# Kernel tuning notes

Hardware: AMD Instinct MI355X
Metric: run time of the kernel (lower is better)

The kernel has to match this reference:

```python
import jax, jax.numpy as jnp
import numpy as np

B, S, D_MODEL = 2, 2048, 2048
H, KVH, HD = 32, 8, 64
N_REP = H // KVH
EPS = 1e-6


def _rope_tables(seq_len, head_dim):
    pos = np.arange(seq_len, dtype=np.float32)
    inv_freq = 1.0 / (10000.0 ** (np.arange(0, head_dim, 2, dtype=np.float32) / head_dim))
    freqs = pos[:, None] * inv_freq[None, :]           # [S, HD/2]
    emb = np.concatenate([freqs, freqs], axis=-1)      # [S, HD]
    return jnp.asarray(np.cos(emb)), jnp.asarray(np.sin(emb))


def setup_inputs() -> dict:
    key = jax.random.key(0)
    ks = jax.random.split(key, 6)
    x = jax.random.normal(ks[0], (B, S, D_MODEL), jnp.float32)
    rope_cos, rope_sin = _rope_tables(S, HD)
    sc_in = 1.0 / np.sqrt(D_MODEL).astype(np.float32)
    sc_o = 1.0 / np.sqrt(H * HD).astype(np.float32)
    Wq = jax.random.normal(ks[1], (H * HD, D_MODEL), jnp.float32) * sc_in
    Wk = jax.random.normal(ks[2], (KVH * HD, D_MODEL), jnp.float32) * sc_in
    Wv = jax.random.normal(ks[3], (KVH * HD, D_MODEL), jnp.float32) * sc_in
    Wo = jax.random.normal(ks[4], (D_MODEL, H * HD), jnp.float32) * sc_o
    q_norm_w = jnp.ones((HD,), jnp.float32)
    k_norm_w = jnp.ones((HD,), jnp.float32)
    return dict(x=x, rope_cos=rope_cos, rope_sin=rope_sin, Wq=Wq, Wk=Wk, Wv=Wv,
                Wo=Wo, q_norm_w=q_norm_w, k_norm_w=k_norm_w)


def _rms_norm(x, w):
    return x * jax.lax.rsqrt(jnp.mean(x * x, axis=-1, keepdims=True) + EPS) * w


def _rotate_half(x):
    x1, x2 = jnp.split(x, 2, axis=-1)
    return jnp.concatenate((-x2, x1), axis=-1)


def reference(x, rope_cos, rope_sin, Wq, Wk, Wv, Wo, q_norm_w, k_norm_w):
    b, s, _ = x.shape
    q = (x @ Wq.T).reshape(b, s, H, HD)
    k = (x @ Wk.T).reshape(b, s, KVH, HD)
    v = (x @ Wv.T).reshape(b, s, KVH, HD)
    # per-head QK RMSNorm
    q = _rms_norm(q, q_norm_w)
    k = _rms_norm(k, k_norm_w)
    # RoPE: cos/sin [S, HD] -> broadcast over heads
    cos = rope_cos[:, None, :]
    sin = rope_sin[:, None, :]
    q = q * cos + _rotate_half(q) * sin
    k = k * cos + _rotate_half(k) * sin
    # GQA: repeat_interleave KV heads
    k = jnp.repeat(k, N_REP, axis=2)
    v = jnp.repeat(v, N_REP, axis=2)
    q = q.transpose(0, 2, 1, 3)  # [B,H,S,HD]
    k = k.transpose(0, 2, 1, 3)
    v = v.transpose(0, 2, 1, 3)
    scale = np.float32(1.0 / np.sqrt(HD))
    scores = jnp.einsum('bhqd,bhkd->bhqk', q, k) * scale
    causal = jnp.tril(jnp.ones((s, s), dtype=bool))
    scores = jnp.where(causal, scores, jnp.finfo(scores.dtype).min)
    attn = jax.nn.softmax(scores, axis=-1)
    out = jnp.einsum('bhqk,bhkd->bhqd', attn, v)
    out = out.transpose(0, 2, 1, 3).reshape(b, s, H * HD)
    return out @ Wo.T
```

## Files before the change

kernel.cpp:

```cpp
#include <hip/hip_runtime.h>
#include <stdint.h>

#define B_ 2
#define S_ 2048
#define DM_ 2048
#define H_ 32
#define KVH_ 8
#define HD_ 64
#define NQK_ 3072

typedef unsigned short u16;
typedef unsigned int u32;
typedef __attribute__((ext_vector_type(8))) short bf16x8;
typedef __attribute__((ext_vector_type(4))) float f32x4;

static __device__ __forceinline__ u16 f2bf(float f) {
  unsigned int u = __float_as_uint(f);
  u = (u + 0x7fffu + ((u >> 16) & 1u)) >> 16;
  return (u16)u;
}
static __device__ __forceinline__ float bf2f(u16 v) {
  unsigned int u = ((unsigned int)v) << 16;
  return __uint_as_float(u);
}

static __device__ __forceinline__ void gload16(const void* g, void* lds_wave_base) {
  __builtin_amdgcn_global_load_lds(
      (__attribute__((address_space(1))) unsigned int*)(uintptr_t)g,
      (__attribute__((address_space(3))) unsigned int*)(uintptr_t)lds_wave_base,
      16, 0, 0);
}

__global__ void cvt_bf16(const float* __restrict__ in, u16* __restrict__ out, int n4) {
  int i = blockIdx.x * blockDim.x + threadIdx.x;
  if (i >= n4) return;
  const float4 v = ((const float4*)in)[i];
  ushort4 o;
  o.x = f2bf(v.x); o.y = f2bf(v.y); o.z = f2bf(v.z); o.w = f2bf(v.w);
  ((ushort4*)out)[i] = o;
}

#define BM 128
#define BN 128
#define BK 32

#define GEMM_BODY(CSTORE)                                                       \
  __shared__ u16 As[2][BM * BK];                                                \
  __shared__ u16 Bs[2][BN * BK];                                                \
  const int t = threadIdx.x;                                                    \
  const int lane = t & 63;                                                      \
  const int w = t >> 6;                                                         \
  const int wr = (w >> 1) * 64, wc = (w & 1) * 64;                              \
  const int m0 = blockIdx.y * BM;                                               \
  const int n0 = blockIdx.x * BN;                                               \
  f32x4 acc[4][4] = {};                                                         \
  const char* Ab = (const char*)A;                                              \
  const char* Bb = (const char*)Bw;                                             \
  const size_t K2 = (size_t)K * 2;                                              \
  const int P0 = t * 16;                                                        \
  const int row0 = P0 >> 6, kb0 = P0 & 63;                                      \
  const int P1 = 4096 + t * 16;                                                 \
  const int row1 = P1 >> 6, kb1 = P1 & 63;                                      \
  const int Pb0 = (w << 10), Pb1 = 4096 + (w << 10);                            \
  auto STAGE = [&](int buf, int k0) {                                           \
    gload16(Ab + (size_t)(m0 + row0) * K2 + (size_t)k0 * 2 + kb0, (char*)As[buf] + Pb0); \
    gload16(Ab + (size_t)(m0 + row1) * K2 + (size_t)k0 * 2 + kb1, (char*)As[buf] + Pb1); \
    gload16(Bb + (size_t)(n0 + row0) * K2 + (size_t)k0 * 2 + kb0, (char*)Bs[buf] + Pb0); \
    gload16(Bb + (size_t)(n0 + row1) * K2 + (size_t)k0 * 2 + kb1, (char*)Bs[buf] + Pb1); \
  };                                                                            \
  STAGE(0, 0);                                                                  \
  __syncthreads();                                                              \
  int cur = 0;                                                                  \
  for (int k0 = 0; k0 < K; k0 += BK) {                                          \
    if (k0 + BK < K) STAGE(cur ^ 1, k0 + BK);                                   \
    bf16x8 af[4], bfr[4];                                                       \
    _Pragma("unroll")                                                           \
    for (int m = 0; m < 4; m++)                                                 \
      af[m] = *(const bf16x8*)((const char*)As[cur] +                           \
               (wr + m * 16 + (lane & 15)) * 64 + ((lane >> 4) << 4));          \
    _Pragma("unroll")                                                           \
    for (int n = 0; n < 4; n++)                                                 \
      bfr[n] = *(const bf16x8*)((const char*)Bs[cur] +                          \
               (wc + n * 16 + (lane & 15)) * 64 + ((lane >> 4) << 4));          \
    _Pragma("unroll")                                                           \
    for (int m = 0; m < 4; m++)                                                 \
      _Pragma("unroll")                                                         \
      for (int n = 0; n < 4; n++)                                               \
        acc[m][n] = __builtin_amdgcn_mfma_f32_16x16x32_bf16(af[m], bfr[n], acc[m][n], 0, 0, 0); \
    __syncthreads();                                                            \
    cur ^= 1;                                                                   \
  }                                                                             \
  _Pragma("unroll")                                                             \
  for (int m = 0; m < 4; m++) {                                                 \
    const int r0 = m0 + wr + m * 16 + ((lane >> 4) << 2);                       \
    _Pragma("unroll")                                                           \
    for (int n = 0; n < 4; n++) {                                               \
      const int c = n0 + wc + n * 16 + (lane & 15);                             \
      _Pragma("unroll")                                                         \
      for (int j = 0; j < 4; j++) CSTORE;                                       \
    }                                                                           \
  }

__global__ __launch_bounds__(256) void gemm_bt(const u16* __restrict__ A,
                                               const u16* __restrict__ Bw,
                                               float* __restrict__ C,
                                               int M, int N, int K) {
  GEMM_BODY(C[(size_t)(r0 + j) * N + c] = acc[m][n][j])
}

__global__ __launch_bounds__(256) void gemm_btb(const u16* __restrict__ A,
                                                const u16* __restrict__ Bw,
                                                u16* __restrict__ C,
                                                int M, int N, int K) {
  GEMM_BODY(C[(size_t)(r0 + j) * N + c] = f2bf(acc[m][n][j]))
}

__global__ void norm_rope_inplace(u16* __restrict__ QKV, const float* __restrict__ cosT,
                                  const float* __restrict__ sinT,
                                  const float* __restrict__ qw,
                                  const float* __restrict__ kw, float qscale) {
  const int r = blockIdx.x * 4 + (threadIdx.x >> 6);
  const int lane = threadIdx.x & 63;
  const int hh2 = r % 40;
  const int bs = r / 40;
  const int s = bs & (S_ - 1);
  const bool isq = hh2 < 32;
  u16* p = QKV + (size_t)bs * NQK_ + hh2 * 64 + lane;
  float x = bf2f(*p);
  float ss = x * x;
#pragma unroll
  for (int m = 1; m < 64; m <<= 1) ss += __shfl_xor(ss, m, 64);
  const float wgt = isq ? qw[lane] : kw[lane];
  float xn = x * rsqrtf(ss * (1.0f / 64.0f) + 1e-6f) * wgt;
  float pr = __shfl_xor(xn, 32, 64);
  float o = xn * cosT[s * 64 + lane] + (lane < 32 ? -pr : pr) * sinT[s * 64 + lane];
  *p = f2bf(o * (isq ? qscale : 1.0f));
}

__global__ void v_transpose(const u16* __restrict__ QKV, u16* __restrict__ Vt) {
  __shared__ u16 tile[64][72];
  const int s0 = blockIdx.x * 64;
  const int bk = blockIdx.y;
  const int b = bk / KVH_, kvh = bk % KVH_;
  const int t = threadIdx.x;
#pragma unroll
  for (int it = 0; it < 16; it++) {
    int idx = it * 256 + t;
    int sl = idx >> 6, d = idx & 63;
    tile[sl][d] = QKV[(size_t)(b * S_ + s0 + sl) * NQK_ + 2560 + kvh * 64 + d];
  }
  __syncthreads();
#pragma unroll
  for (int it = 0; it < 16; it++) {
    int idx = it * 256 + t;
    int d = idx >> 6, sl = idx & 63;
    Vt[(((size_t)(b * KVH_ + kvh)) * HD_ + d) * S_ + s0 + sl] = tile[sl][d];
  }
}

__global__ __launch_bounds__(256, 4) void attn_fwd(const u16* __restrict__ QKV,
                                                   const u16* __restrict__ Vt,
                                                   u16* __restrict__ Out) {
  __shared__ u16 Ksm[2][64 * 64];
  __shared__ u16 Vsm[2][64 * 64];
  __shared__ u16 Psm[4][16 * 64];

  const int t = threadIdx.x, lane = t & 63, w = t >> 6;
  const int q = lane & 15, g = lane >> 4;

  const int fid = blockIdx.y * 16 + blockIdx.x;
  const int xcd = fid & 7, slot = fid >> 3;
  const int kg = xcd * 2 + (slot >> 6);
  const int sub = slot & 63;
  const int ip = sub >> 2;
  const int b = kg >> 3, kvh = kg & 7;
  const int h = kvh * 4 + (sub & 3);

  const char* Kb = (const char*)(QKV + (size_t)b * S_ * NQK_ + 2048 + kvh * 64);
  const char* Vb = (const char*)(Vt + ((size_t)(b * KVH_ + kvh)) * HD_ * S_);

  const int SP0 = t * 16, SP1 = 4096 + t * 16;
  const int srow0 = SP0 >> 7, scb0 = (SP0 ^ ((srow0 & 7) << 4)) & 127;
  const int srow1 = SP1 >> 7, scb1 = (SP1 ^ ((srow1 & 7) << 4)) & 127;
  const int SB0 = (w << 10), SB1 = 4096 + (w << 10);
  const size_t KROW = (size_t)NQK_ * 2;

  auto STAGE = [&](int buf, int kt) {
    gload16(Kb + (size_t)(kt * 64 + srow0) * KROW + scb0, (char*)Ksm[buf] + SB0);
    gload16(Kb + (size_t)(kt * 64 + srow1) * KROW + scb1, (char*)Ksm[buf] + SB1);
    gload16(Vb + (size_t)srow0 * (S_ * 2) + (size_t)kt * 128 + scb0, (char*)Vsm[buf] + SB0);
    gload16(Vb + (size_t)srow1 * (S_ * 2) + (size_t)kt * 128 + scb1, (char*)Vsm[buf] + SB1);
  };

  const int swz = (q & 7) << 4;
  int koff[4][2], voff[4][2], pwoff[4][2], proff[2];
#pragma unroll
  for (int nt = 0; nt < 4; nt++)
#pragma unroll
    for (int hh = 0; hh < 2; hh++) {
      koff[nt][hh] = ((nt * 16 + q) * 128 + hh * 64 + g * 16) ^ swz;
      voff[nt][hh] = ((nt * 16 + q) * 128 + hh * 64 + g * 16) ^ swz;
      pwoff[nt][hh] = (q * 128 + nt * 32 + g * 8 + hh * 4) ^ swz;
    }
#pragma unroll
  for (int c = 0; c < 2; c++) proff[c] = (q * 128 + c * 64 + g * 16) ^ swz;

  bf16x8 ones;
#pragma unroll
  for (int j = 0; j < 8; j++) ones[j] = (short)0x3F80;

  auto process = [&](int qt) {
    const int q0w = qt * 64 + w * 16;
    bf16x8 aq[2];
    {
      const u16* qp = QKV + (size_t)(b * S_ + q0w + q) * NQK_ + h * 64 + g * 8;
      aq[0] = *(const bf16x8*)qp;
      aq[1] = *(const bf16x8*)(qp + 32);
    }
    f32x4 o_acc[4] = {};
    f32x4 l_acc = {};
    float m_i = -1e30f;

    STAGE(0, 0);
    __syncthreads();
    int cur = 0;

    for (int kt = 0; kt <= qt; kt++) {
      if (kt < qt) STAGE(cur ^ 1, kt + 1);

      f32x4 sc[4];
      __builtin_amdgcn_s_setprio(1);
#pragma unroll
      for (int nt = 0; nt < 4; nt++) {
        f32x4 s = {};
#pragma unroll
        for (int hh = 0; hh < 2; hh++) {
          bf16x8 bk = *(const bf16x8*)((const char*)Ksm[cur] + koff[nt][hh]);
          s = __builtin_amdgcn_mfma_f32_16x16x32_bf16(bk, aq[hh], s, 0, 0, 0);
        }
        sc[nt] = s;
      }
      __builtin_amdgcn_s_setprio(0);

      if (kt == qt) {
#pragma unroll
        for (int nt = 0; nt < 4; nt++)
#pragma unroll
          for (int r = 0; r < 4; r++)
            if (nt * 16 + g * 4 + r > w * 16 + q) sc[nt][r] = -1e30f;
      }

      float mx;
      {
        float m0 = fmaxf(fmaxf(sc[0][0], sc[0][1]), fmaxf(sc[0][2], sc[0][3]));
        float m1 = fmaxf(fmaxf(sc[1][0], sc[1][1]), fmaxf(sc[1][2], sc[1][3]));
        float m2 = fmaxf(fmaxf(sc[2][0], sc[2][1]), fmaxf(sc[2][2], sc[2][3]));
        float m3 = fmaxf(fmaxf(sc[3][0], sc[3][1]), fmaxf(sc[3][2], sc[3][3]));
        mx = fmaxf(fmaxf(m0, m1), fmaxf(m2, m3));
      }
      mx = fmaxf(mx, __shfl_xor(mx, 16, 64));
      mx = fmaxf(mx, __shfl_xor(mx, 32, 64));

      if (!__all(mx <= m_i + 8.0f)) {
        const float mn = fmaxf(m_i, mx);
        const float a = exp2f(m_i - mn);
        m_i = mn;
        float aT[4];
#pragma unroll
        for (int r = 0; r < 4; r++)
          aT[r] = __shfl(a, (lane & 48) + ((lane & 48) >> 2) + r, 64);
#pragma unroll
        for (int r = 0; r < 4; r++) {
          l_acc[r] *= aT[r];
#pragma unroll
          for (int dt = 0; dt < 4; dt++) o_acc[dt][r] *= aT[r];
        }
      }

#pragma unroll
      for (int nt = 0; nt < 4; nt++)
#pragma unroll
        for (int r = 0; r < 4; r++) sc[nt][r] = exp2f(sc[nt][r] - m_i);
#pragma unroll
      for (int nt = 0; nt < 4; nt++)
#pragma unroll
        for (int hh = 0; hh < 2; hh++) {
          u32 wv;
          asm("v_cvt_pk_bf16_f32 %0, %1, %2"
              : "=v"(wv) : "v"(sc[nt][2 * hh]), "v"(sc[nt][2 * hh + 1]));
          *(u32*)((char*)Psm[w] + pwoff[nt][hh]) = wv;
        }

      asm volatile("s_waitcnt lgkmcnt(0)" ::: "memory");
      __builtin_amdgcn_sched_barrier(0);

      bf16x8 pa[2];
#pragma unroll
      for (int c = 0; c < 2; c++)
        pa[c] = *(const bf16x8*)((const char*)Psm[w] + proff[c]);

      __builtin_amdgcn_s_setprio(1);
      l_acc = __builtin_amdgcn_mfma_f32_16x16x32_bf16(pa[0], ones, l_acc, 0, 0, 0);
      l_acc = __builtin_amdgcn_mfma_f32_16x16x32_bf16(pa[1], ones, l_acc, 0, 0, 0);
#pragma unroll
      for (int c = 0; c < 2; c++)
#pragma unroll
        for (int dt = 0; dt < 4; dt++) {
          bf16x8 bv = *(const bf16x8*)((const char*)Vsm[cur] + voff[dt][c]);
          o_acc[dt] = __builtin_amdgcn_mfma_f32_16x16x32_bf16(pa[c], bv, o_acc[dt], 0, 0, 0);
        }
      __builtin_amdgcn_s_setprio(0);

      __syncthreads();
      cur ^= 1;
    }

#pragma unroll
    for (int r = 0; r < 4; r++) {
      const int qg = q0w + g * 4 + r;
      const float inv = 1.0f / l_acc[r];
#pragma unroll
      for (int dt = 0; dt < 4; dt++)
        Out[(((size_t)b * S_ + qg) * H_ + h) * HD_ + dt * 16 + q] =
            f2bf(o_acc[dt][r] * inv);
    }
  };

  process(ip);
  process(31 - ip);
}

extern "C" void kernel_launch(void* const* d_in, const int* in_sizes, int n_in,
                              void* d_out, int out_size, void* d_ws, size_t ws_size,
                              hipStream_t stream) {
  const float* x  = (const float*)d_in[0];
  const float* rc = (const float*)d_in[1];
  const float* rs = (const float*)d_in[2];
  const float* Wq = (const float*)d_in[3];
  const float* Wk = (const float*)d_in[4];
  const float* Wv = (const float*)d_in[5];
  const float* Wo = (const float*)d_in[6];
  const float* qw = (const float*)d_in[7];
  const float* kw = (const float*)d_in[8];
  float* out = (float*)d_out;

  char* ws = (char*)d_ws;
  const size_t MB = (size_t)1 << 20;
  u16* xb   = (u16*)(ws + 0 * MB);
  u16* wbq  = (u16*)(ws + 16 * MB);
  u16* QKVb = (u16*)(ws + 28 * MB);
  u16* Vtb  = (u16*)(ws + 52 * MB);
  u16* AO   = xb;

  const int MT = B_ * S_;
  const float QSC = 0.125f * 1.44269504089f;

  cvt_bf16<<<dim3(MT * DM_ / 1024), 256, 0, stream>>>(x, xb, MT * DM_ / 4);
  cvt_bf16<<<dim3(DM_ * DM_ / 1024), 256, 0, stream>>>(Wq, wbq, DM_ * DM_ / 4);
  cvt_bf16<<<dim3(512 * DM_ / 1024), 256, 0, stream>>>(Wk, wbq + (size_t)DM_ * DM_, 512 * DM_ / 4);
  cvt_bf16<<<dim3(512 * DM_ / 1024), 256, 0, stream>>>(Wv, wbq + (size_t)DM_ * DM_ + (size_t)512 * DM_, 512 * DM_ / 4);

  gemm_btb<<<dim3(NQK_ / BN, MT / BM), 256, 0, stream>>>(xb, wbq, QKVb, MT, NQK_, DM_);

  norm_rope_inplace<<<dim3(MT * 40 / 4), 256, 0, stream>>>(QKVb, rc, rs, qw, kw, QSC);

  v_transpose<<<dim3(S_ / 64, B_ * KVH_), 256, 0, stream>>>(QKVb, Vtb);

  attn_fwd<<<dim3(16, 64), 256, 0, stream>>>(QKVb, Vtb, AO);

  cvt_bf16<<<dim3(DM_ * DM_ / 1024), 256, 0, stream>>>(Wo, wbq, DM_ * DM_ / 4);
  gemm_bt<<<dim3(DM_ / BN, MT / BM), 256, 0, stream>>>(AO, wbq, out, MT, DM_, DM_);
}
```

Before: 240.1 us.

## Restructure attention to 32x32 MFMA with paired lo/hi query tiles sharing K/V loads

The attention kernel now uses 32x32x16 MFMAs, giving each wave 32 query rows instead of 16. Each block processes a low and a high causal query tile together in one pass, so every staged K/V tile serves both. The P matrix is rearranged in registers with v_permlane32_swap instead of a round trip through LDS. The grid shrinks to 512 blocks with launch bounds of 2, trading occupancy and register pressure for fewer K/V loads and no LDS traffic for P.

```diff
diff --git a/kernel.cpp b/kernel.cpp
--- a/kernel.cpp
+++ b/kernel.cpp
@@ -13,6 +13,8 @@
 typedef unsigned int u32;
 typedef __attribute__((ext_vector_type(8))) short bf16x8;
 typedef __attribute__((ext_vector_type(4))) float f32x4;
+typedef __attribute__((ext_vector_type(16))) float f32x16;
+typedef __attribute__((ext_vector_type(4))) u32 u32x4;
 
 static __device__ __forceinline__ u16 f2bf(float f) {
   unsigned int u = __float_as_uint(f);
@@ -158,23 +160,28 @@
   }
 }
 
-__global__ __launch_bounds__(256, 4) void attn_fwd(const u16* __restrict__ QKV,
+__global__ __launch_bounds__(256, 2) void attn_fwd(const u16* __restrict__ QKV,
                                                    const u16* __restrict__ Vt,
                                                    u16* __restrict__ Out) {
   __shared__ u16 Ksm[2][64 * 64];
   __shared__ u16 Vsm[2][64 * 64];
-  __shared__ u16 Psm[4][16 * 64];
 
   const int t = threadIdx.x, lane = t & 63, w = t >> 6;
-  const int q = lane & 15, g = lane >> 4;
-
-  const int fid = blockIdx.y * 16 + blockIdx.x;
+  const int q31 = lane & 31, hi = lane >> 5;
+
+  const int fid = blockIdx.x;
   const int xcd = fid & 7, slot = fid >> 3;
-  const int kg = xcd * 2 + (slot >> 6);
-  const int sub = slot & 63;
-  const int ip = sub >> 2;
+  const int kg = xcd * 2 + (slot >> 5);
+  const int sub = slot & 31;
   const int b = kg >> 3, kvh = kg & 7;
   const int h = kvh * 4 + (sub & 3);
+  const int ip = sub >> 2;
+
+  const int qlo0 = ip * 128 + w * 32;
+  const int qhi0 = (15 - ip) * 128 + w * 32;
+  const int ktlo_max = (qlo0 + 31) >> 6;
+  const int kthi_max = (qhi0 + 31) >> 6;
+  const int KT = (15 - ip) * 2 + 1;
 
   const char* Kb = (const char*)(QKV + (size_t)b * S_ * NQK_ + 2048 + kvh * 64);
   const char* Vb = (const char*)(Vt + ((size_t)(b * KVH_ + kvh)) * HD_ * S_);
@@ -192,142 +199,169 @@
     gload16(Vb + (size_t)srow1 * (S_ * 2) + (size_t)kt * 128 + scb1, (char*)Vsm[buf] + SB1);
   };
 
-  const int swz = (q & 7) << 4;
-  int koff[4][2], voff[4][2], pwoff[4][2], proff[2];
-#pragma unroll
-  for (int nt = 0; nt < 4; nt++)
-#pragma unroll
-    for (int hh = 0; hh < 2; hh++) {
-      koff[nt][hh] = ((nt * 16 + q) * 128 + hh * 64 + g * 16) ^ swz;
-      voff[nt][hh] = ((nt * 16 + q) * 128 + hh * 64 + g * 16) ^ swz;
-      pwoff[nt][hh] = (q * 128 + nt * 32 + g * 8 + hh * 4) ^ swz;
-    }
-#pragma unroll
-  for (int c = 0; c < 2; c++) proff[c] = (q * 128 + c * 64 + g * 16) ^ swz;
+  bf16x8 qf0[4], qf1[4];
+  {
+    const u16* qp0 = QKV + (size_t)(b * S_ + qlo0 + q31) * NQK_ + h * 64 + hi * 8;
+    const u16* qp1 = QKV + (size_t)(b * S_ + qhi0 + q31) * NQK_ + h * 64 + hi * 8;
+#pragma unroll
+    for (int sl = 0; sl < 4; sl++) {
+      qf0[sl] = *(const bf16x8*)(qp0 + sl * 16);
+      qf1[sl] = *(const bf16x8*)(qp1 + sl * 16);
+    }
+  }
 
   bf16x8 ones;
 #pragma unroll
   for (int j = 0; j < 8; j++) ones[j] = (short)0x3F80;
 
-  auto process = [&](int qt) {
-    const int q0w = qt * 64 + w * 16;
-    bf16x8 aq[2];
+  f32x16 o00 = {}, o01 = {}, o10 = {}, o11 = {};
+  f32x16 l0 = {}, l1 = {};
+  float m0 = -1e30f, m1 = -1e30f;
+
+  auto cvtpk = [](float a, float bb) {
+    u32 r;
+    asm("v_cvt_pk_bf16_f32 %0, %1, %2" : "=v"(r) : "v"(a), "v"(bb));
+    return r;
+  };
+
+  STAGE(0, 0);
+  __syncthreads();
+  int cur = 0;
+
+  for (int kt = 0; kt <= KT; kt++) {
+    if (kt < KT) STAGE(cur ^ 1, kt + 1);
+
+    bf16x8 kf[2][4];
+#pragma unroll
+    for (int kh = 0; kh < 2; kh++)
+#pragma unroll
+      for (int sl = 0; sl < 4; sl++) {
+        const int row = kh * 32 + q31;
+        const int byt = (row * 128 + sl * 32 + hi * 16) ^ ((row & 7) << 4);
+        kf[kh][sl] = *(const bf16x8*)((const char*)Ksm[cur] + byt);
+      }
+
+    bf16x8 pa0[4], pa1[4];
+    const bool act0 = (kt <= ktlo_max);
+    const bool act1 = (kt <= kthi_max);
+
+#define QTILE(ACT, QF, PA, MI, LI, OA, OB, Q0, KTMAX)                           \
+    if (ACT) {                                                                  \
+      f32x16 p0 = {}, p1 = {};                                                  \
+      __builtin_amdgcn_s_setprio(1);                                            \
+      _Pragma("unroll")                                                         \
+      for (int sl = 0; sl < 4; sl++) {                                          \
+        p0 = __builtin_amdgcn_mfma_f32_32x32x16_bf16(kf[0][sl], QF[sl], p0, 0, 0, 0); \
+        p1 = __builtin_amdgcn_mfma_f32_32x32x16_bf16(kf[1][sl], QF[sl], p1, 0, 0, 0); \
+      }                                                                         \
+      __builtin_amdgcn_s_setprio(0);                                            \
+      if (kt == KTMAX) {                                                        \
+        const int qg = Q0 + q31;                                                \
+        _Pragma("unroll")                                                       \
+        for (int r = 0; r < 16; r++) {                                          \
+          const int crow = (r & 3) + 8 * (r >> 2) + 4 * hi;                     \
+          if (kt * 64 + crow > qg) p0[r] = -1e30f;                              \
+          if (kt * 64 + 32 + crow > qg) p1[r] = -1e30f;                         \
+        }                                                                       \
+      }                                                                         \
+      float mx = fmaxf(p0[0], p1[0]);                                           \
+      _Pragma("unroll")                                                         \
+      for (int r = 1; r < 16; r++) mx = fmaxf(mx, fmaxf(p0[r], p1[r]));         \
+      mx = fmaxf(mx, __shfl_xor(mx, 32, 64));                                   \
+      if (!__all(mx <= MI + 8.0f)) {                                            \
+        const float mn = fmaxf(MI, mx);                                         \
+        const float al = exp2f(MI - mn);                                        \
+        MI = mn;                                                                \
+        _Pragma("unroll")                                                       \
+        for (int r = 0; r < 16; r++) {                                          \
+          const float aO = __shfl(al, (r & 3) + 8 * (r >> 2) + 4 * hi, 64);     \
+          LI[r] *= aO; OA[r] *= aO; OB[r] *= aO;                                \
+        }                                                                       \
+      }                                                                         \
+      _Pragma("unroll")                                                         \
+      for (int r = 0; r < 16; r++) {                                            \
+        p0[r] = exp2f(p0[r] - MI);                                              \
+        p1[r] = exp2f(p1[r] - MI);                                              \
+      }                                                                         \
+      u32 wa, wb2, wc2, wd;                                                     \
+      union { u32x4 u; bf16x8 h; } cv;                                          \
+      wa = cvtpk(p0[0], p0[1]);  wb2 = cvtpk(p0[2], p0[3]);                     \
+      wc2 = cvtpk(p0[4], p0[5]); wd = cvtpk(p0[6], p0[7]);                      \
+      asm("v_permlane32_swap_b32 %0, %1" : "+v"(wa), "+v"(wc2));                \
+      asm("v_permlane32_swap_b32 %0, %1" : "+v"(wb2), "+v"(wd));                \
+      cv.u[0] = wa; cv.u[1] = wb2; cv.u[2] = wc2; cv.u[3] = wd; PA[0] = cv.h;   \
+      wa = cvtpk(p0[8], p0[9]);   wb2 = cvtpk(p0[10], p0[11]);                  \
+      wc2 = cvtpk(p0[12], p0[13]); wd = cvtpk(p0[14], p0[15]);                  \
+      asm("v_permlane32_swap_b32 %0, %1" : "+v"(wa), "+v"(wc2));                \
+      asm("v_permlane32_swap_b32 %0, %1" : "+v"(wb2), "+v"(wd));                \
+      cv.u[0] = wa; cv.u[1] = wb2; cv.u[2] = wc2; cv.u[3] = wd; PA[1] = cv.h;   \
+      wa = cvtpk(p1[0], p1[1]);  wb2 = cvtpk(p1[2], p1[3]);                     \
+      wc2 = cvtpk(p1[4], p1[5]); wd = cvtpk(p1[6], p1[7]);                      \
+      asm("v_permlane32_swap_b32 %0, %1" : "+v"(wa), "+v"(wc2));                \
+      asm("v_permlane32_swap_b32 %0, %1" : "+v"(wb2), "+v"(wd));                \
+      cv.u[0] = wa; cv.u[1] = wb2; cv.u[2] = wc2; cv.u[3] = wd; PA[2] = cv.h;   \
+      wa = cvtpk(p1[8], p1[9]);   wb2 = cvtpk(p1[10], p1[11]);                  \
+      wc2 = cvtpk(p1[12], p1[13]); wd = cvtpk(p1[14], p1[15]);                  \
+      asm("v_permlane32_swap_b32 %0, %1" : "+v"(wa), "+v"(wc2));                \
+      asm("v_permlane32_swap_b32 %0, %1" : "+v"(wb2), "+v"(wd));                \
+      cv.u[0] = wa; cv.u[1] = wb2; cv.u[2] = wc2; cv.u[3] = wd; PA[3] = cv.h;   \
+    }
+
+    QTILE(act0, qf0, pa0, m0, l0, o00, o01, qlo0, ktlo_max)
+    QTILE(act1, qf1, pa1, m1, l1, o10, o11, qhi0, kthi_max)
+#undef QTILE
+
+    bf16x8 vf[4][2];
+#pragma unroll
+    for (int sl = 0; sl < 4; sl++)
+#pragma unroll
+      for (int dt = 0; dt < 2; dt++) {
+        const int row = dt * 32 + q31;
+        const int byt = (row * 128 + sl * 32 + hi * 16) ^ ((row & 7) << 4);
+        vf[sl][dt] = *(const bf16x8*)((const char*)Vsm[cur] + byt);
+      }
+
+    __builtin_amdgcn_s_setprio(1);
+    if (act0) {
+#pragma unroll
+      for (int sl = 0; sl < 4; sl++) {
+        l0 = __builtin_amdgcn_mfma_f32_32x32x16_bf16(pa0[sl], ones, l0, 0, 0, 0);
+        o00 = __builtin_amdgcn_mfma_f32_32x32x16_bf16(pa0[sl], vf[sl][0], o00, 0, 0, 0);
+        o01 = __builtin_amdgcn_mfma_f32_32x32x16_bf16(pa0[sl], vf[sl][1], o01, 0, 0, 0);
+      }
+    }
+    if (act1) {
+#pragma unroll
+      for (int sl = 0; sl < 4; sl++) {
+        l1 = __builtin_amdgcn_mfma_f32_32x32x16_bf16(pa1[sl], ones, l1, 0, 0, 0);
+        o10 = __builtin_amdgcn_mfma_f32_32x32x16_bf16(pa1[sl], vf[sl][0], o10, 0, 0, 0);
+        o11 = __builtin_amdgcn_mfma_f32_32x32x16_bf16(pa1[sl], vf[sl][1], o11, 0, 0, 0);
+      }
+    }
+    __builtin_amdgcn_s_setprio(0);
+
+    __syncthreads();
+    cur ^= 1;
+  }
+
+#pragma unroll
+  for (int r = 0; r < 16; r++) {
+    const int crow = (r & 3) + 8 * (r >> 2) + 4 * hi;
     {
-      const u16* qp = QKV + (size_t)(b * S_ + q0w + q) * NQK_ + h * 64 + g * 8;
-      aq[0] = *(const bf16x8*)qp;
-      aq[1] = *(const bf16x8*)(qp + 32);
-    }
-    f32x4 o_acc[4] = {};
-    f32x4 l_acc = {};
-    float m_i = -1e30f;
-
-    STAGE(0, 0);
-    __syncthreads();
-    int cur = 0;
-
-    for (int kt = 0; kt <= qt; kt++) {
-      if (kt < qt) STAGE(cur ^ 1, kt + 1);
-
-      f32x4 sc[4];
-      __builtin_amdgcn_s_setprio(1);
-#pragma unroll
-      for (int nt = 0; nt < 4; nt++) {
-        f32x4 s = {};
-#pragma unroll
-        for (int hh = 0; hh < 2; hh++) {
-          bf16x8 bk = *(const bf16x8*)((const char*)Ksm[cur] + koff[nt][hh]);
-          s = __builtin_amdgcn_mfma_f32_16x16x32_bf16(bk, aq[hh], s, 0, 0, 0);
-        }
-        sc[nt] = s;
-      }
-      __builtin_amdgcn_s_setprio(0);
-
-      if (kt == qt) {
-#pragma unroll
-        for (int nt = 0; nt < 4; nt++)
-#pragma unroll
-          for (int r = 0; r < 4; r++)
-            if (nt * 16 + g * 4 + r > w * 16 + q) sc[nt][r] = -1e30f;
-      }
-
-      float mx;
-      {
-        float m0 = fmaxf(fmaxf(sc[0][0], sc[0][1]), fmaxf(sc[0][2], sc[0][3]));
-        float m1 = fmaxf(fmaxf(sc[1][0], sc[1][1]), fmaxf(sc[1][2], sc[1][3]));
-        float m2 = fmaxf(fmaxf(sc[2][0], sc[2][1]), fmaxf(sc[2][2], sc[2][3]));
-        float m3 = fmaxf(fmaxf(sc[3][0], sc[3][1]), fmaxf(sc[3][2], sc[3][3]));
-        mx = fmaxf(fmaxf(m0, m1), fmaxf(m2, m3));
-      }
-      mx = fmaxf(mx, __shfl_xor(mx, 16, 64));
-      mx = fmaxf(mx, __shfl_xor(mx, 32, 64));
-
-      if (!__all(mx <= m_i + 8.0f)) {
-        const float mn = fmaxf(m_i, mx);
-        const float a = exp2f(m_i - mn);
-        m_i = mn;
-        float aT[4];
-#pragma unroll
-        for (int r = 0; r < 4; r++)
-          aT[r] = __shfl(a, (lane & 48) + ((lane & 48) >> 2) + r, 64);
-#pragma unroll
-        for (int r = 0; r < 4; r++) {
-          l_acc[r] *= aT[r];
-#pragma unroll
-          for (int dt = 0; dt < 4; dt++) o_acc[dt][r] *= aT[r];
-        }
-      }
-
-#pragma unroll
-      for (int nt = 0; nt < 4; nt++)
-#pragma unroll
-        for (int r = 0; r < 4; r++) sc[nt][r] = exp2f(sc[nt][r] - m_i);
-#pragma unroll
-      for (int nt = 0; nt < 4; nt++)
-#pragma unroll
-        for (int hh = 0; hh < 2; hh++) {
-          u32 wv;
-          asm("v_cvt_pk_bf16_f32 %0, %1, %2"
-              : "=v"(wv) : "v"(sc[nt][2 * hh]), "v"(sc[nt][2 * hh + 1]));
-          *(u32*)((char*)Psm[w] + pwoff[nt][hh]) = wv;
-        }
-
-      asm volatile("s_waitcnt lgkmcnt(0)" ::: "memory");
-      __builtin_amdgcn_sched_barrier(0);
-
-      bf16x8 pa[2];
-#pragma unroll
-      for (int c = 0; c < 2; c++)
-        pa[c] = *(const bf16x8*)((const char*)Psm[w] + proff[c]);
-
-      __builtin_amdgcn_s_setprio(1);
-      l_acc = __builtin_amdgcn_mfma_f32_16x16x32_bf16(pa[0], ones, l_acc, 0, 0, 0);
-      l_acc = __builtin_amdgcn_mfma_f32_16x16x32_bf16(pa[1], ones, l_acc, 0, 0, 0);
-#pragma unroll
-      for (int c = 0; c < 2; c++)
-#pragma unroll
-        for (int dt = 0; dt < 4; dt++) {
-          bf16x8 bv = *(const bf16x8*)((const char*)Vsm[cur] + voff[dt][c]);
-          o_acc[dt] = __builtin_amdgcn_mfma_f32_16x16x32_bf16(pa[c], bv, o_acc[dt], 0, 0, 0);
-        }
-      __builtin_amdgcn_s_setprio(0);
-
-      __syncthreads();
-      cur ^= 1;
-    }
-
-#pragma unroll
-    for (int r = 0; r < 4; r++) {
-      const int qg = q0w + g * 4 + r;
-      const float inv = 1.0f / l_acc[r];
-#pragma unroll
-      for (int dt = 0; dt < 4; dt++)
-        Out[(((size_t)b * S_ + qg) * H_ + h) * HD_ + dt * 16 + q] =
-            f2bf(o_acc[dt][r] * inv);
-    }
-  };
-
-  process(ip);
-  process(31 - ip);
+      const int qg = qlo0 + crow;
+      const float inv = 1.0f / l0[r];
+      u16* op = Out + (((size_t)(b * S_ + qg)) * H_ + h) * HD_;
+      op[q31] = f2bf(o00[r] * inv);
+      op[32 + q31] = f2bf(o01[r] * inv);
+    }
+    {
+      const int qg = qhi0 + crow;
+      const float inv = 1.0f / l1[r];
+      u16* op = Out + (((size_t)(b * S_ + qg)) * H_ + h) * HD_;
+      op[q31] = f2bf(o10[r] * inv);
+      op[32 + q31] = f2bf(o11[r] * inv);
+    }
+  }
 }
 
 extern "C" void kernel_launch(void* const* d_in, const int* in_sizes, int n_in,
@@ -366,7 +400,7 @@
 
   v_transpose<<<dim3(S_ / 64, B_ * KVH_), 256, 0, stream>>>(QKVb, Vtb);
 
-  attn_fwd<<<dim3(16, 64), 256, 0, stream>>>(QKVb, Vtb, AO);
+  attn_fwd<<<dim3(512), 256, 0, stream>>>(QKVb, Vtb, AO);
 
   cvt_bf16<<<dim3(DM_ * DM_ / 1024), 256, 0, stream>>>(Wo, wbq, DM_ * DM_ / 4);
   gemm_bt<<<dim3(DM_ / BN, MT / BM), 256, 0, stream>>>(AO, wbq, out, MT, DM_, DM_);
```

Result: no change. 240.3 us (+0.1%).

## Rewrite attention with 32x32 MFMA, split-KV waves and register-resident P

Applied to the files above, without the earlier changes.

The attention kernel moves from 16x16x32 to 32x32x16 MFMAs, with each wave owning a 32-row query tile and half of each 64-key block (two waves per query tile split along keys). P is converted to the MFMA operand layout in registers using v_permlane32_swap instead of a round trip through LDS, and row sums are computed with shuffles instead of a ones-MFMA. The two key-halves are merged at the end through shared memory. Each block now handles one query slab instead of a paired short+long slab, so the grid doubles and load balancing relies on scheduling longest slabs first. This trades an extra end-of-block reduction and half-idle waves on the diagonal block for fewer LDS operations and larger MFMA tiles.

```diff
diff --git a/kernel.cpp b/kernel.cpp
--- a/kernel.cpp
+++ b/kernel.cpp
@@ -13,6 +13,8 @@
 typedef unsigned int u32;
 typedef __attribute__((ext_vector_type(8))) short bf16x8;
 typedef __attribute__((ext_vector_type(4))) float f32x4;
+typedef __attribute__((ext_vector_type(16))) float f32x16;
+typedef __attribute__((ext_vector_type(4))) u32 u32x4;
 
 static __device__ __forceinline__ u16 f2bf(float f) {
   unsigned int u = __float_as_uint(f);
@@ -163,18 +165,21 @@
                                                    u16* __restrict__ Out) {
   __shared__ u16 Ksm[2][64 * 64];
   __shared__ u16 Vsm[2][64 * 64];
-  __shared__ u16 Psm[4][16 * 64];
 
   const int t = threadIdx.x, lane = t & 63, w = t >> 6;
-  const int q = lane & 15, g = lane >> 4;
-
-  const int fid = blockIdx.y * 16 + blockIdx.x;
+  const int q31 = lane & 31, hi = lane >> 5;
+  const int tile_r = w & 1, kside = w >> 1;
+
+  const int fid = blockIdx.x;
   const int xcd = fid & 7, slot = fid >> 3;
-  const int kg = xcd * 2 + (slot >> 6);
-  const int sub = slot & 63;
-  const int ip = sub >> 2;
+  const int kg = xcd * 2 + (slot >> 7);
+  const int sub = slot & 127;
   const int b = kg >> 3, kvh = kg & 7;
   const int h = kvh * 4 + (sub & 3);
+  const int slab = 31 - (sub >> 2);
+
+  const int q0 = slab * 64 + tile_r * 32;
+  const int KTM = slab;
 
   const char* Kb = (const char*)(QKV + (size_t)b * S_ * NQK_ + 2048 + kvh * 64);
   const char* Vb = (const char*)(Vt + ((size_t)(b * KVH_ + kvh)) * HD_ * S_);
@@ -192,142 +197,146 @@
     gload16(Vb + (size_t)srow1 * (S_ * 2) + (size_t)kt * 128 + scb1, (char*)Vsm[buf] + SB1);
   };
 
-  const int swz = (q & 7) << 4;
-  int koff[4][2], voff[4][2], pwoff[4][2], proff[2];
-#pragma unroll
-  for (int nt = 0; nt < 4; nt++)
-#pragma unroll
-    for (int hh = 0; hh < 2; hh++) {
-      koff[nt][hh] = ((nt * 16 + q) * 128 + hh * 64 + g * 16) ^ swz;
-      voff[nt][hh] = ((nt * 16 + q) * 128 + hh * 64 + g * 16) ^ swz;
-      pwoff[nt][hh] = (q * 128 + nt * 32 + g * 8 + hh * 4) ^ swz;
-    }
-#pragma unroll
-  for (int c = 0; c < 2; c++) proff[c] = (q * 128 + c * 64 + g * 16) ^ swz;
-
-  bf16x8 ones;
-#pragma unroll
-  for (int j = 0; j < 8; j++) ones[j] = (short)0x3F80;
-
-  auto process = [&](int qt) {
-    const int q0w = qt * 64 + w * 16;
-    bf16x8 aq[2];
-    {
-      const u16* qp = QKV + (size_t)(b * S_ + q0w + q) * NQK_ + h * 64 + g * 8;
-      aq[0] = *(const bf16x8*)qp;
-      aq[1] = *(const bf16x8*)(qp + 32);
-    }
-    f32x4 o_acc[4] = {};
-    f32x4 l_acc = {};
-    float m_i = -1e30f;
-
-    STAGE(0, 0);
-    __syncthreads();
-    int cur = 0;
-
-    for (int kt = 0; kt <= qt; kt++) {
-      if (kt < qt) STAGE(cur ^ 1, kt + 1);
-
-      f32x4 sc[4];
+  STAGE(0, 0);
+
+  bf16x8 qf[4];
+  {
+    const u16* qp = QKV + (size_t)(b * S_ + q0 + q31) * NQK_ + h * 64 + hi * 8;
+#pragma unroll
+    for (int sl = 0; sl < 4; sl++) qf[sl] = *(const bf16x8*)(qp + sl * 16);
+  }
+
+  f32x16 o0 = {}, o1 = {};
+  float m_i = -1e30f, l_i = 0.0f;
+
+  auto cvtpk = [](float a, float bb) {
+    u32 r;
+    asm("v_cvt_pk_bf16_f32 %0, %1, %2" : "=v"(r) : "v"(a), "v"(bb));
+    return r;
+  };
+
+  const int swz = (q31 & 7) << 4;
+  __syncthreads();
+  int cur = 0;
+
+  for (int kt = 0; kt <= KTM; kt++) {
+    if (kt < KTM) STAGE(cur ^ 1, kt + 1);
+
+    const bool act = (kt < KTM) || (kside <= tile_r);
+    if (act) {
+      f32x16 p = {};
       __builtin_amdgcn_s_setprio(1);
 #pragma unroll
-      for (int nt = 0; nt < 4; nt++) {
-        f32x4 s = {};
-#pragma unroll
-        for (int hh = 0; hh < 2; hh++) {
-          bf16x8 bk = *(const bf16x8*)((const char*)Ksm[cur] + koff[nt][hh]);
-          s = __builtin_amdgcn_mfma_f32_16x16x32_bf16(bk, aq[hh], s, 0, 0, 0);
+      for (int sl = 0; sl < 4; sl++) {
+        const int byt = ((kside * 32 + q31) * 128 + sl * 32 + hi * 16) ^ swz;
+        bf16x8 kf = *(const bf16x8*)((const char*)Ksm[cur] + byt);
+        p = __builtin_amdgcn_mfma_f32_32x32x16_bf16(kf, qf[sl], p, 0, 0, 0);
+      }
+      __builtin_amdgcn_s_setprio(0);
+
+      if (kt == KTM) {
+        const int rel = tile_r * 32 + q31 - kside * 32;
+#pragma unroll
+        for (int r = 0; r < 16; r++) {
+          const int crow = (r & 3) + 8 * (r >> 2) + 4 * hi;
+          if (crow > rel) p[r] = -1e30f;
         }
-        sc[nt] = s;
-      }
-      __builtin_amdgcn_s_setprio(0);
-
-      if (kt == qt) {
-#pragma unroll
-        for (int nt = 0; nt < 4; nt++)
-#pragma unroll
-          for (int r = 0; r < 4; r++)
-            if (nt * 16 + g * 4 + r > w * 16 + q) sc[nt][r] = -1e30f;
-      }
-
-      float mx;
-      {
-        float m0 = fmaxf(fmaxf(sc[0][0], sc[0][1]), fmaxf(sc[0][2], sc[0][3]));
-        float m1 = fmaxf(fmaxf(sc[1][0], sc[1][1]), fmaxf(sc[1][2], sc[1][3]));
-        float m2 = fmaxf(fmaxf(sc[2][0], sc[2][1]), fmaxf(sc[2][2], sc[2][3]));
-        float m3 = fmaxf(fmaxf(sc[3][0], sc[3][1]), fmaxf(sc[3][2], sc[3][3]));
-        mx = fmaxf(fmaxf(m0, m1), fmaxf(m2, m3));
-      }
-      mx = fmaxf(mx, __shfl_xor(mx, 16, 64));
+      }
+
+      float a0 = fmaxf(p[0], p[1]),  a1 = fmaxf(p[2], p[3]);
+      float a2 = fmaxf(p[4], p[5]),  a3 = fmaxf(p[6], p[7]);
+      float a4 = fmaxf(p[8], p[9]),  a5 = fmaxf(p[10], p[11]);
+      float a6 = fmaxf(p[12], p[13]), a7 = fmaxf(p[14], p[15]);
+      float mx = fmaxf(fmaxf(fmaxf(a0, a1), fmaxf(a2, a3)),
+                       fmaxf(fmaxf(a4, a5), fmaxf(a6, a7)));
       mx = fmaxf(mx, __shfl_xor(mx, 32, 64));
 
       if (!__all(mx <= m_i + 8.0f)) {
         const float mn = fmaxf(m_i, mx);
-        const float a = exp2f(m_i - mn);
+        const float al = exp2f(m_i - mn);
         m_i = mn;
-        float aT[4];
-#pragma unroll
-        for (int r = 0; r < 4; r++)
-          aT[r] = __shfl(a, (lane & 48) + ((lane & 48) >> 2) + r, 64);
-#pragma unroll
-        for (int r = 0; r < 4; r++) {
-          l_acc[r] *= aT[r];
-#pragma unroll
-          for (int dt = 0; dt < 4; dt++) o_acc[dt][r] *= aT[r];
+        l_i *= al;
+#pragma unroll
+        for (int r = 0; r < 16; r++) {
+          const float aO = __shfl(al, (r & 3) + 8 * (r >> 2) + 4 * hi, 64);
+          o0[r] *= aO;
+          o1[r] *= aO;
         }
       }
 
-#pragma unroll
-      for (int nt = 0; nt < 4; nt++)
-#pragma unroll
-        for (int r = 0; r < 4; r++) sc[nt][r] = exp2f(sc[nt][r] - m_i);
-#pragma unroll
-      for (int nt = 0; nt < 4; nt++)
-#pragma unroll
-        for (int hh = 0; hh < 2; hh++) {
-          u32 wv;
-          asm("v_cvt_pk_bf16_f32 %0, %1, %2"
-              : "=v"(wv) : "v"(sc[nt][2 * hh]), "v"(sc[nt][2 * hh + 1]));
-          *(u32*)((char*)Psm[w] + pwoff[nt][hh]) = wv;
-        }
-
-      asm volatile("s_waitcnt lgkmcnt(0)" ::: "memory");
-      __builtin_amdgcn_sched_barrier(0);
+      float rs = 0.0f;
+#pragma unroll
+      for (int r = 0; r < 16; r++) {
+        p[r] = exp2f(p[r] - m_i);
+        rs += p[r];
+      }
+      rs += __shfl_xor(rs, 32, 64);
+      l_i += rs;
 
       bf16x8 pa[2];
-#pragma unroll
-      for (int c = 0; c < 2; c++)
-        pa[c] = *(const bf16x8*)((const char*)Psm[w] + proff[c]);
+      {
+        u32 wa, wb2, wc2, wd;
+        union { u32x4 u; bf16x8 hh; } cv;
+        wa = cvtpk(p[0], p[1]);   wb2 = cvtpk(p[2], p[3]);
+        wc2 = cvtpk(p[4], p[5]);  wd = cvtpk(p[6], p[7]);
+        asm("v_permlane32_swap_b32 %0, %1" : "+v"(wa), "+v"(wc2));
+        asm("v_permlane32_swap_b32 %0, %1" : "+v"(wb2), "+v"(wd));
+        cv.u[0] = wa; cv.u[1] = wb2; cv.u[2] = wc2; cv.u[3] = wd; pa[0] = cv.hh;
+        wa = cvtpk(p[8], p[9]);    wb2 = cvtpk(p[10], p[11]);
+        wc2 = cvtpk(p[12], p[13]); wd = cvtpk(p[14], p[15]);
+        asm("v_permlane32_swap_b32 %0, %1" : "+v"(wa), "+v"(wc2));
+        asm("v_permlane32_swap_b32 %0, %1" : "+v"(wb2), "+v"(wd));
+        cv.u[0] = wa; cv.u[1] = wb2; cv.u[2] = wc2; cv.u[3] = wd; pa[1] = cv.hh;
+      }
 
       __builtin_amdgcn_s_setprio(1);
-      l_acc = __builtin_amdgcn_mfma_f32_16x16x32_bf16(pa[0], ones, l_acc, 0, 0, 0);
-      l_acc = __builtin_amdgcn_mfma_f32_16x16x32_bf16(pa[1], ones, l_acc, 0, 0, 0);
-#pragma unroll
-      for (int c = 0; c < 2; c++)
-#pragma unroll
-        for (int dt = 0; dt < 4; dt++) {
-          bf16x8 bv = *(const bf16x8*)((const char*)Vsm[cur] + voff[dt][c]);
-          o_acc[dt] = __builtin_amdgcn_mfma_f32_16x16x32_bf16(pa[c], bv, o_acc[dt], 0, 0, 0);
-        }
+#pragma unroll
+      for (int j = 0; j < 2; j++) {
+        const int colb = kside * 64 + j * 32 + hi * 16;
+        bf16x8 v0 = *(const bf16x8*)((const char*)Vsm[cur] +
+                     ((q31 * 128 + colb) ^ swz));
+        bf16x8 v1 = *(const bf16x8*)((const char*)Vsm[cur] +
+                     (((32 + q31) * 128 + colb) ^ swz));
+        o0 = __builtin_amdgcn_mfma_f32_32x32x16_bf16(pa[j], v0, o0, 0, 0, 0);
+        o1 = __builtin_amdgcn_mfma_f32_32x32x16_bf16(pa[j], v1, o1, 0, 0, 0);
+      }
       __builtin_amdgcn_s_setprio(0);
-
-      __syncthreads();
-      cur ^= 1;
     }
 
-#pragma unroll
-    for (int r = 0; r < 4; r++) {
-      const int qg = q0w + g * 4 + r;
-      const float inv = 1.0f / l_acc[r];
-#pragma unroll
-      for (int dt = 0; dt < 4; dt++)
-        Out[(((size_t)b * S_ + qg) * H_ + h) * HD_ + dt * 16 + q] =
-            f2bf(o_acc[dt][r] * inv);
+    __syncthreads();
+    cur ^= 1;
+  }
+
+  float* smo = (float*)Ksm;
+  float* smlm = (float*)Vsm;
+  if (kside == 1) {
+    float* dst = smo + tile_r * 2048 + lane * 32;
+#pragma unroll
+    for (int r = 0; r < 16; r++) { dst[r] = o0[r]; dst[16 + r] = o1[r]; }
+    smlm[tile_r * 128 + lane * 2] = l_i;
+    smlm[tile_r * 128 + lane * 2 + 1] = m_i;
+  }
+  __syncthreads();
+  if (kside == 0) {
+    const float lB = smlm[tile_r * 128 + lane * 2];
+    const float mB = smlm[tile_r * 128 + lane * 2 + 1];
+    const float m12 = fmaxf(m_i, mB);
+    const float aA = exp2f(m_i - m12);
+    const float aB = exp2f(mB - m12);
+    const float linv = 1.0f / (l_i * aA + lB * aB);
+    const float* src = smo + tile_r * 2048 + lane * 32;
+#pragma unroll
+    for (int r = 0; r < 16; r++) {
+      const int crow = (r & 3) + 8 * (r >> 2) + 4 * hi;
+      const float fA = __shfl(aA, crow, 64);
+      const float fB = __shfl(aB, crow, 64);
+      const float fl = __shfl(linv, crow, 64);
+      const int qg = q0 + crow;
+      u16* op = Out + (((size_t)(b * S_ + qg)) * H_ + h) * HD_;
+      op[q31] = f2bf((o0[r] * fA + src[r] * fB) * fl);
+      op[32 + q31] = f2bf((o1[r] * fA + src[16 + r] * fB) * fl);
     }
-  };
-
-  process(ip);
-  process(31 - ip);
+  }
 }
 
 extern "C" void kernel_launch(void* const* d_in, const int* in_sizes, int n_in,
@@ -366,7 +375,7 @@
 
   v_transpose<<<dim3(S_ / 64, B_ * KVH_), 256, 0, stream>>>(QKVb, Vtb);
 
-  attn_fwd<<<dim3(16, 64), 256, 0, stream>>>(QKVb, Vtb, AO);
+  attn_fwd<<<dim3(2048), 256, 0, stream>>>(QKVb, Vtb, AO);
 
   cvt_bf16<<<dim3(DM_ * DM_ / 1024), 256, 0, stream>>>(Wo, wbq, DM_ * DM_ / 4);
   gemm_bt<<<dim3(DM_ / BN, MT / BM), 256, 0, stream>>>(AO, wbq, out, MT, DM_, DM_);
```

Result: slower. 247.4 us (+3.0%).

## Replace GEMM with 128x256 tile, 8-wave, triple-buffered swizzled LDS pipeline

Applied to the files above, without the earlier changes.

Replaces the double-buffered 128x128x32 GEMM with a 512-thread kernel that computes 128x256 tiles with BK=64. It uses three LDS buffers with XOR-swizzled rows to avoid bank conflicts, explicit vmcnt waits and barriers to interleave prefetch with MFMA quadrants, s_setprio around the MFMA blocks, and an XCD-aware block remapping. The aim is higher arithmetic intensity and better overlap of global loads with MFMA in the QKV and output projections. In exchange the kernel hardcodes K=2048, uses about 144KB of LDS, and its hand-scheduled waitcnt logic is fragile.

```diff
diff --git a/kernel.cpp b/kernel.cpp
--- a/kernel.cpp
+++ b/kernel.cpp
@@ -8,6 +8,8 @@
 #define KVH_ 8
 #define HD_ 64
 #define NQK_ 3072
+#define GK 2048
+#define NT 32
 
 typedef unsigned short u16;
 typedef unsigned int u32;
@@ -40,79 +42,126 @@
   ((ushort4*)out)[i] = o;
 }
 
-#define BM 128
-#define BN 128
-#define BK 32
-
-#define GEMM_BODY(CSTORE)                                                       \
-  __shared__ u16 As[2][BM * BK];                                                \
-  __shared__ u16 Bs[2][BN * BK];                                                \
-  const int t = threadIdx.x;                                                    \
-  const int lane = t & 63;                                                      \
-  const int w = t >> 6;                                                         \
-  const int wr = (w >> 1) * 64, wc = (w & 1) * 64;                              \
-  const int m0 = blockIdx.y * BM;                                               \
-  const int n0 = blockIdx.x * BN;                                               \
-  f32x4 acc[4][4] = {};                                                         \
-  const char* Ab = (const char*)A;                                              \
-  const char* Bb = (const char*)Bw;                                             \
-  const size_t K2 = (size_t)K * 2;                                              \
-  const int P0 = t * 16;                                                        \
-  const int row0 = P0 >> 6, kb0 = P0 & 63;                                      \
-  const int P1 = 4096 + t * 16;                                                 \
-  const int row1 = P1 >> 6, kb1 = P1 & 63;                                      \
-  const int Pb0 = (w << 10), Pb1 = 4096 + (w << 10);                            \
-  auto STAGE = [&](int buf, int k0) {                                           \
-    gload16(Ab + (size_t)(m0 + row0) * K2 + (size_t)k0 * 2 + kb0, (char*)As[buf] + Pb0); \
-    gload16(Ab + (size_t)(m0 + row1) * K2 + (size_t)k0 * 2 + kb1, (char*)As[buf] + Pb1); \
-    gload16(Bb + (size_t)(n0 + row0) * K2 + (size_t)k0 * 2 + kb0, (char*)Bs[buf] + Pb0); \
-    gload16(Bb + (size_t)(n0 + row1) * K2 + (size_t)k0 * 2 + kb1, (char*)Bs[buf] + Pb1); \
-  };                                                                            \
-  STAGE(0, 0);                                                                  \
-  __syncthreads();                                                              \
-  int cur = 0;                                                                  \
-  for (int k0 = 0; k0 < K; k0 += BK) {                                          \
-    if (k0 + BK < K) STAGE(cur ^ 1, k0 + BK);                                   \
-    bf16x8 af[4], bfr[4];                                                       \
-    _Pragma("unroll")                                                           \
-    for (int m = 0; m < 4; m++)                                                 \
-      af[m] = *(const bf16x8*)((const char*)As[cur] +                           \
-               (wr + m * 16 + (lane & 15)) * 64 + ((lane >> 4) << 4));          \
-    _Pragma("unroll")                                                           \
-    for (int n = 0; n < 4; n++)                                                 \
-      bfr[n] = *(const bf16x8*)((const char*)Bs[cur] +                          \
-               (wc + n * 16 + (lane & 15)) * 64 + ((lane >> 4) << 4));          \
-    _Pragma("unroll")                                                           \
-    for (int m = 0; m < 4; m++)                                                 \
-      _Pragma("unroll")                                                         \
-      for (int n = 0; n < 4; n++)                                               \
-        acc[m][n] = __builtin_amdgcn_mfma_f32_16x16x32_bf16(af[m], bfr[n], acc[m][n], 0, 0, 0); \
-    __syncthreads();                                                            \
-    cur ^= 1;                                                                   \
-  }                                                                             \
-  _Pragma("unroll")                                                             \
-  for (int m = 0; m < 4; m++) {                                                 \
-    const int r0 = m0 + wr + m * 16 + ((lane >> 4) << 2);                       \
-    _Pragma("unroll")                                                           \
-    for (int n = 0; n < 4; n++) {                                               \
-      const int c = n0 + wc + n * 16 + (lane & 15);                             \
-      _Pragma("unroll")                                                         \
-      for (int j = 0; j < 4; j++) CSTORE;                                       \
+#define LOADFRAG(BUF, MH, NH)                                                   \
+  do {                                                                          \
+    const char* bufA = lds + (BUF) * 49152;                                     \
+    const char* bufB = bufA + 16384;                                            \
+    _Pragma("unroll") for (int i = 0; i < 2; i++)                               \
+    _Pragma("unroll") for (int kk = 0; kk < 2; kk++) {                          \
+      const int ra = wr + (2 * (MH) + i) * 16 + q;                              \
+      af[i][kk] = *(const bf16x8*)(bufA + ra * 128 +                            \
+                   ((kk * 64 + g * 16) ^ ((ra & 7) << 4)));                     \
+      const int rb = wc + (2 * (NH) + i) * 16 + q;                              \
+      bfv[i][kk] = *(const bf16x8*)(bufB + rb * 128 +                           \
+                   ((kk * 64 + g * 16) ^ ((rb & 7) << 4)));                     \
     }                                                                           \
+  } while (0)
+
+#define MFMAQ(MH, NH)                                                           \
+  do {                                                                          \
+    __builtin_amdgcn_s_setprio(1);                                              \
+    _Pragma("unroll") for (int i = 0; i < 2; i++)                               \
+    _Pragma("unroll") for (int j = 0; j < 2; j++)                               \
+    _Pragma("unroll") for (int kk = 0; kk < 2; kk++)                            \
+      acc[2 * (MH) + i][2 * (NH) + j] = __builtin_amdgcn_mfma_f32_16x16x32_bf16(\
+          af[i][kk], bfv[j][kk], acc[2 * (MH) + i][2 * (NH) + j], 0, 0, 0);     \
+    __builtin_amdgcn_s_setprio(0);                                              \
+  } while (0)
+
+#define GBAR() asm volatile("s_barrier" ::: "memory")
+
+template <bool BF16OUT>
+__global__ __launch_bounds__(512, 2) void gemm8(const u16* __restrict__ A,
+                                                const u16* __restrict__ Bw,
+                                                void* __restrict__ Cv,
+                                                int M, int N) {
+  __shared__ char lds[3 * 49152];
+  const int t = threadIdx.x, lane = t & 63, w = t >> 6;
+  const int q = lane & 15, g = lane >> 4;
+
+  const int cpx = gridDim.x >> 3;
+  const int wg = (blockIdx.x & 7) * cpx + (blockIdx.x >> 3);
+  const int nbx = N >> 8;
+  const int bx = wg % nbx, by = wg / nbx;
+  const int m0 = by * 128, n0 = bx * 256;
+  const int wr = (w >> 2) * 64, wc = (w & 3) * 64;
+
+  const char* Ab = (const char*)A;
+  const char* Bb = (const char*)Bw;
+  const size_t K2 = (size_t)GK * 2;
+
+  f32x4 acc[4][4] = {};
+
+  const int P0 = t * 16, P1 = 8192 + t * 16;
+  const int r0s = P0 >> 7, c0s = (P0 & 127) ^ ((r0s & 7) << 4);
+  const int r1s = P1 >> 7, c1s = (P1 & 127) ^ ((r1s & 7) << 4);
+
+  auto stA = [&](int buf, int kt) {
+    char* d = lds + buf * 49152;
+    gload16(Ab + (size_t)(m0 + r0s) * K2 + kt * 128 + c0s, d + (w << 10));
+    gload16(Ab + (size_t)(m0 + r1s) * K2 + kt * 128 + c1s, d + 8192 + (w << 10));
+  };
+  auto stB = [&](int buf, int half, int kt) {
+    char* d = lds + buf * 49152 + 16384 + half * 16384;
+    gload16(Bb + (size_t)(n0 + half * 128 + r0s) * K2 + kt * 128 + c0s, d + (w << 10));
+    gload16(Bb + (size_t)(n0 + half * 128 + r1s) * K2 + kt * 128 + c1s, d + 8192 + (w << 10));
+  };
+
+  stA(0, 0); stB(0, 0, 0); stB(0, 1, 0);
+  stA(1, 1); stB(1, 0, 1); stB(1, 1, 1);
+
+  for (int kt = 0; kt < NT; kt++) {
+    const int cb_ = kt % 3;
+    const int nb = (kt + 2) % 3;
+    const bool pf = (kt + 2 < NT);
+    bf16x8 af[2][2], bfv[2][2];
+
+    if (pf) stA(nb, kt + 2);
+    if (kt < NT - 2) {
+      asm volatile("s_waitcnt vmcnt(8)" ::: "memory");
+    } else if (kt == NT - 2) {
+      asm volatile("s_waitcnt vmcnt(6)" ::: "memory");
+    } else {
+      asm volatile("s_waitcnt vmcnt(0)" ::: "memory");
+    }
+    GBAR();
+    LOADFRAG(cb_, 0, 0);
+    MFMAQ(0, 0);
+    GBAR();
+
+    LOADFRAG(cb_, 1, 0);
+    if (pf) stB(nb, 0, kt + 2);
+    GBAR();
+    MFMAQ(1, 0);
+    GBAR();
+
+    LOADFRAG(cb_, 0, 1);
+    if (pf) stB(nb, 1, kt + 2);
+    GBAR();
+    MFMAQ(0, 1);
+    GBAR();
+
+    LOADFRAG(cb_, 1, 1);
+    GBAR();
+    MFMAQ(1, 1);
+    GBAR();
   }
 
-__global__ __launch_bounds__(256) void gemm_bt(const u16* __restrict__ A,
-                                               const u16* __restrict__ Bw,
-                                               float* __restrict__ C,
-                                               int M, int N, int K) {
-  GEMM_BODY(C[(size_t)(r0 + j) * N + c] = acc[m][n][j])
-}
-
-__global__ __launch_bounds__(256) void gemm_btb(const u16* __restrict__ A,
-                                                const u16* __restrict__ Bw,
-                                                u16* __restrict__ C,
-                                                int M, int N, int K) {
-  GEMM_BODY(C[(size_t)(r0 + j) * N + c] = f2bf(acc[m][n][j]))
+#pragma unroll
+  for (int m = 0; m < 4; m++) {
+    const int r0 = m0 + wr + m * 16 + g * 4;
+#pragma unroll
+    for (int n = 0; n < 4; n++) {
+      const int c = n0 + wc + n * 16 + q;
+#pragma unroll
+      for (int j = 0; j < 4; j++) {
+        if constexpr (BF16OUT)
+          ((u16*)Cv)[(size_t)(r0 + j) * N + c] = f2bf(acc[m][n][j]);
+        else
+          ((float*)Cv)[(size_t)(r0 + j) * N + c] = acc[m][n][j];
+      }
+    }
+  }
 }
 
 __global__ void norm_rope_inplace(u16* __restrict__ QKV, const float* __restrict__ cosT,
@@ -360,7 +409,7 @@
   cvt_bf16<<<dim3(512 * DM_ / 1024), 256, 0, stream>>>(Wk, wbq + (size_t)DM_ * DM_, 512 * DM_ / 4);
   cvt_bf16<<<dim3(512 * DM_ / 1024), 256, 0, stream>>>(Wv, wbq + (size_t)DM_ * DM_ + (size_t)512 * DM_, 512 * DM_ / 4);
 
-  gemm_btb<<<dim3(NQK_ / BN, MT / BM), 256, 0, stream>>>(xb, wbq, QKVb, MT, NQK_, DM_);
+  gemm8<true><<<dim3(384), 512, 0, stream>>>(xb, wbq, QKVb, MT, NQK_);
 
   norm_rope_inplace<<<dim3(MT * 40 / 4), 256, 0, stream>>>(QKVb, rc, rs, qw, kw, QSC);
 
@@ -369,5 +418,5 @@
   attn_fwd<<<dim3(16, 64), 256, 0, stream>>>(QKVb, Vtb, AO);
 
   cvt_bf16<<<dim3(DM_ * DM_ / 1024), 256, 0, stream>>>(Wo, wbq, DM_ * DM_ / 4);
-  gemm_bt<<<dim3(DM_ / BN, MT / BM), 256, 0, stream>>>(AO, wbq, out, MT, DM_, DM_);
-}
+  gemm8<false><<<dim3(256), 512, 0, stream>>>(AO, wbq, out, MT, DM_);
+}
```

Result: slower. 258.2 us (+7.5%).
